# Kernel tuning notes

Measured on AMD Instinct MI355X. Metric: run time of the kernel, lower is better.

Reference implementation:

```python
import jax, jax.numpy as jnp
import numpy as np

TOPK = 180          # init kwarg topk
TOL = 3             # init kwarg tolerance_px


def setup_inputs() -> dict:
    key = jax.random.key(0)
    k1, k2, k3 = jax.random.split(key, 3)
    shape = (32, 1, 512, 512)
    return {
        "rv": jax.random.normal(k1, shape, dtype=jnp.float32),
        "ri": jax.random.normal(k2, shape, dtype=jnp.float32),
        "rf": jax.random.normal(k3, shape, dtype=jnp.float32),
    }


def reference(rv, ri, rf):
    # rf already matches rv spatially, so the interpolate branch is a no-op.
    b, c, h, w = rv.shape
    n = c * h * w
    rv_flat = rv.reshape(b, n)
    ri_flat = ri.reshape(b, n)
    rf_flat = rf.reshape(b, n)

    k = min(TOPK, n)
    _, rv_idx = jax.lax.top_k(rv_flat, k)                 # [b, k]
    _, ri_idx = jax.lax.top_k(ri_flat, k)                 # [b, k]
    _, rf_idx = jax.lax.top_k(rf_flat, min(2 * k, n))     # [b, 2k]

    rows = jnp.arange(b)[:, None]
    # union mask of VIS+IR keypoints (scatter 1.0 at top-k indices)
    src_mask = (
        jnp.zeros((b, n), jnp.float32)
        .at[rows, rv_idx].set(1.0)
        .at[rows, ri_idx].set(1.0)
    )
    src_mask = (src_mask > 0).astype(jnp.float32).reshape(b, c, h, w)

    fused_mask = (
        jnp.zeros((b, n), jnp.float32).at[rows, rf_idx].set(1.0)
    ).reshape(b, c, h, w)

    if TOL > 0:
        ksz = 2 * TOL + 1
        # max_pool2d(kernel=ksz, stride=1, padding=TOL) == dilation of the mask
        fused_mask = jax.lax.reduce_window(
            fused_mask, -jnp.inf, jax.lax.max,
            window_dimensions=(1, 1, ksz, ksz),
            window_strides=(1, 1, 1, 1),
            padding=[(0, 0), (0, 0), (TOL, TOL), (TOL, TOL)],
        )

    fused_hit = (fused_mask > 0).astype(jnp.float32)
    cover = (src_mask * fused_hit).reshape(b, -1).sum(axis=1)
    denom = jnp.maximum(src_mask.reshape(b, -1).sum(axis=1), 1.0)
    coverage = cover / denom
    return (1.0 - coverage).mean()
```

## Files before the change

### kernel.cpp

```cpp
#include <hip/hip_runtime.h>

#define N_ELEM 262144
#define SPLIT 32
#define NTS 256
#define SLICE_CAP 256
#define LSEL 2048
#define TIE_CAP 512
#define THRESH 2.5f

__device__ __forceinline__ unsigned keyOf(float f) {
    unsigned u = __float_as_uint(f);
    return (u & 0x80000000u) ? ~u : (u | 0x80000000u);
}

__device__ __forceinline__ const float* pairSrc(int p, const float* rv, const float* ri, const float* rf) {
    int t = p % 3, b = p / 3;
    return (t == 0 ? rv : (t == 1 ? ri : rf)) + (size_t)b * N_ELEM;
}

__global__ __launch_bounds__(NTS) void collect_kernel(const float* __restrict__ rv,
                                                      const float* __restrict__ ri,
                                                      const float* __restrict__ rf,
                                                      int* __restrict__ cntS,
                                                      unsigned long long* __restrict__ cand,
                                                      float* __restrict__ out,
                                                      int* __restrict__ done, int B) {
    const int p = blockIdx.x / SPLIT;
    const int s = blockIdx.x % SPLIT;
    const float4* p4 = (const float4*)pairSrc(p, rv, ri, rf) + (size_t)s * (N_ELEM / 4 / SPLIT);

    __shared__ unsigned long long buf[SLICE_CAP];
    __shared__ int s_m;
    const int tid = threadIdx.x;

    if (blockIdx.x == 0) {
        if (tid < B) done[tid] = 0;
        if (tid == B) *out = 0.0f;
    }
    if (tid == 0) s_m = 0;
    __syncthreads();

    const int base_idx = s * (N_ELEM / SPLIT);
    for (int i = tid; i < N_ELEM / 4 / SPLIT; i += NTS) {
        float4 v = p4[i];
        int pos;
        if (v.x > THRESH) { pos = atomicAdd(&s_m, 1); if (pos < SLICE_CAP) buf[pos] = ((unsigned long long)keyOf(v.x) << 32) | (unsigned)(base_idx + 4 * i + 0); }
        if (v.y > THRESH) { pos = atomicAdd(&s_m, 1); if (pos < SLICE_CAP) buf[pos] = ((unsigned long long)keyOf(v.y) << 32) | (unsigned)(base_idx + 4 * i + 1); }
        if (v.z > THRESH) { pos = atomicAdd(&s_m, 1); if (pos < SLICE_CAP) buf[pos] = ((unsigned long long)keyOf(v.z) << 32) | (unsigned)(base_idx + 4 * i + 2); }
        if (v.w > THRESH) { pos = atomicAdd(&s_m, 1); if (pos < SLICE_CAP) buf[pos] = ((unsigned long long)keyOf(v.w) << 32) | (unsigned)(base_idx + 4 * i + 3); }
    }
    __syncthreads();

    int m = s_m;
    const bool over = (m > SLICE_CAP);
    if (over) m = SLICE_CAP;
    if (tid == 0) cntS[p * SPLIT + s] = over ? -1 : m;
    unsigned long long* my = cand + (size_t)(p * SPLIT + s) * SLICE_CAP;
    for (int i = tid; i < m; i += NTS) my[i] = buf[i];
}

__global__ __launch_bounds__(NTS) void select_cov_kernel(const float* __restrict__ rv,
                                                         const float* __restrict__ ri,
                                                         const float* __restrict__ rf,
                                                         const int* __restrict__ cntS,
                                                         const unsigned long long* __restrict__ cand,
                                                         int* __restrict__ idx_out,
                                                         int* __restrict__ done,
                                                         float* __restrict__ out,
                                                         float inv_b) {
    const int p = blockIdx.x;
    const int t = p % 3;
    const int bb = p / 3;
    const int K = (t == 2) ? 360 : 180;
    int* obuf = idx_out + (size_t)p * 360;
    const int tid = threadIdx.x;

    __shared__ __align__(16) unsigned char smem[49152];
    unsigned* lcKey = (unsigned*)smem;
    unsigned* lcIdx = (unsigned*)(smem + 8192);
    __shared__ unsigned hist[256];
    __shared__ int ties[TIE_CAP];
    __shared__ int soff[SPLIT]; __shared__ int scnt[SPLIT];
    __shared__ int s_total, s_bad;
    __shared__ unsigned s_p2; __shared__ int s_b2; __shared__ int s_cg2;
    __shared__ int s_on, s_tn, s_pickd; __shared__ unsigned s_pickb;
    __shared__ int s_prev, s_u, s_c;

    if (tid < 64) {
        int c = (tid < SPLIT) ? cntS[p * SPLIT + tid] : 0;
        int bad = (c < 0) ? 1 : 0;
        int cc = bad ? 0 : c;
        int v = cc;
        #pragma unroll
        for (int off = 1; off < 64; off <<= 1) {
            int u = __shfl_up(v, off, 64);
            if (tid >= off) v += u;
        }
        if (tid < SPLIT) { soff[tid] = v - cc; scnt[tid] = cc; }
        if (tid == 63) s_total = v;
        unsigned long long bm = __ballot(bad != 0);
        if (tid == 0) s_bad = (bm != 0ull) ? 1 : 0;
    }
    __syncthreads();
    const int total = s_total;
    const bool fits = (!s_bad) && (total >= K) && (total <= LSEL);

    if (fits) {
        const int sl = tid >> 3;
        const int j0 = tid & 7;
        const unsigned long long* src = cand + (size_t)(p * SPLIT + sl) * SLICE_CAP;
        const int c = scnt[sl];
        const int o = soff[sl];
        for (int j = j0; j < c; j += 8) {
            unsigned long long e = src[j];
            lcKey[o + j] = (unsigned)(e >> 32);
            lcIdx[o + j] = (unsigned)(e & 0xffffffffu);
        }
    }
    __syncthreads();

    const float4* p4 = (const float4*)pairSrc(p, rv, ri, rf);

    if (tid == 0) { s_p2 = 0; s_b2 = 0; s_cg2 = 0; }
    __syncthreads();

    while (s_b2 < 32) {
        hist[tid] = 0;
        __syncthreads();
        {
            const int b2 = s_b2; const unsigned p2 = s_p2;
            const int sh2 = 24 - b2;
            if (fits) {
                for (int i = tid; i < total; i += NTS) {
                    unsigned kk = lcKey[i];
                    bool match = (b2 == 0) || ((kk >> (32 - b2)) == p2);
                    if (match) atomicAdd(&hist[(kk >> sh2) & 255u], 1u);
                }
            } else {
                for (int i = tid; i < N_ELEM / 4; i += NTS) {
                    float4 v = p4[i];
                    unsigned kk;
                    kk = keyOf(v.x); if ((b2 == 0) || ((kk >> (32 - b2)) == p2)) atomicAdd(&hist[(kk >> sh2) & 255u], 1u);
                    kk = keyOf(v.y); if ((b2 == 0) || ((kk >> (32 - b2)) == p2)) atomicAdd(&hist[(kk >> sh2) & 255u], 1u);
                    kk = keyOf(v.z); if ((b2 == 0) || ((kk >> (32 - b2)) == p2)) atomicAdd(&hist[(kk >> sh2) & 255u], 1u);
                    kk = keyOf(v.w); if ((b2 == 0) || ((kk >> (32 - b2)) == p2)) atomicAdd(&hist[(kk >> sh2) & 255u], 1u);
                }
            }
        }
        __syncthreads();
        const unsigned r = (unsigned)(K - s_cg2);
        if (tid < 64) {
            const int l = tid;
            unsigned h0 = hist[4*l+0], h1 = hist[4*l+1], h2 = hist[4*l+2], h3 = hist[4*l+3];
            unsigned sum4 = h0 + h1 + h2 + h3;
            unsigned suf = sum4;
            #pragma unroll
            for (int off = 1; off < 64; off <<= 1) {
                unsigned u = __shfl_down(suf, off, 64);
                if (l + off < 64) suf += u;
            }
            unsigned s0 = suf, s1 = s0 - h0, s2 = s1 - h1, s3 = s2 - h2, s4 = s3 - h3;
            int d = -1; unsigned below = 0;
            if      (s3 >= r && s4 < r) { d = 4*l+3; below = s4; }
            else if (s2 >= r && s3 < r) { d = 4*l+2; below = s3; }
            else if (s1 >= r && s2 < r) { d = 4*l+1; below = s2; }
            else if (s0 >= r && s1 < r) { d = 4*l+0; below = s1; }
            if (d >= 0) { s_pickd = d; s_pickb = below; }
        }
        __syncthreads();
        if (tid == 0) {
            s_p2 = (s_p2 << 8) | (unsigned)s_pickd;
            s_cg2 += (int)s_pickb;
            s_b2 += 8;
        }
        __syncthreads();
    }

    if (tid == 0) { s_on = 0; s_tn = 0; }
    __syncthreads();

    {
        const unsigned Kth = s_p2;
        if (fits) {
            for (int i = tid; i < total; i += NTS) {
                unsigned kk = lcKey[i];
                int idx = (int)lcIdx[i];
                if (kk > Kth) { int pos = atomicAdd(&s_on, 1); obuf[pos] = idx; }
                else if (kk == Kth) { int pos = atomicAdd(&s_tn, 1); if (pos < TIE_CAP) ties[pos] = idx; }
            }
        } else {
            for (int i = tid; i < N_ELEM / 4; i += NTS) {
                float4 v = p4[i];
                float vals[4] = {v.x, v.y, v.z, v.w};
                for (int c = 0; c < 4; ++c) {
                    unsigned kk = keyOf(vals[c]);
                    if (kk > Kth) { int pos = atomicAdd(&s_on, 1); obuf[pos] = 4 * i + c; }
                    else if (kk == Kth) { int pos = atomicAdd(&s_tn, 1); if (pos < TIE_CAP) ties[pos] = 4 * i + c; }
                }
            }
        }
    }
    __syncthreads();
    if (tid == 0) {
        int need = K - s_cg2;
        int tn = s_tn; if (tn > TIE_CAP) tn = TIE_CAP;
        int rr = need; if (rr > tn) rr = tn;
        for (int a = 0; a < rr; ++a) {
            int mb = a;
            for (int j = a + 1; j < tn; ++j) if (ties[j] < ties[mb]) mb = j;
            int tmp = ties[a]; ties[a] = ties[mb]; ties[mb] = tmp;
            obuf[s_on + a] = ties[a];
        }
        for (int a = rr; a < need; ++a) obuf[s_on + a] = (tn > 0) ? ties[0] : 0;
    }

    __threadfence();
    __syncthreads();
    if (tid == 0) s_prev = atomicAdd(&done[bb], 1);
    __syncthreads();
    if (s_prev == 2) {
        __threadfence();
        unsigned* rfbm  = (unsigned*)smem;
        unsigned* srcbm = (unsigned*)(smem + 32768);
        const int* rvI = idx_out + (size_t)(bb * 3 + 0) * 360;
        const int* riI = idx_out + (size_t)(bb * 3 + 1) * 360;
        const int* rfI = idx_out + (size_t)(bb * 3 + 2) * 360;

        for (int i = tid; i < 8192; i += NTS) rfbm[i] = 0;
        if (tid == 0) { s_u = 0; s_c = 0; }
        __syncthreads();
        for (int i = tid; i < 360; i += NTS) {
            int v = rfI[i];
            atomicOr(&rfbm[v >> 5], 1u << (v & 31));
        }
        __syncthreads();

        int myu = 0, myc = 0;
        for (int h = 0; h < 2; ++h) {
            for (int i = tid; i < 4096; i += NTS) srcbm[i] = 0;
            __syncthreads();
            for (int i = tid; i < 360; i += NTS) {
                int v = (i < 180) ? rvI[i] : riI[i - 180];
                int y = v >> 9, x = v & 511;
                if ((y >> 8) == h) {
                    unsigned bit = 1u << (v & 31);
                    unsigned old = atomicOr(&srcbm[(v >> 5) & 4095], bit);
                    if (!(old & bit)) {
                        myu++;
                        int lo = x - 3; if (lo < 0) lo = 0;
                        int hi = x + 3; if (hi > 511) hi = 511;
                        int k0 = lo >> 5, k1 = hi >> 5;
                        unsigned m0, m1;
                        if (k0 == k1) { m0 = ((1u << (hi - lo + 1)) - 1u) << (lo & 31); m1 = 0u; }
                        else          { m0 = 0xffffffffu << (lo & 31); m1 = (1u << ((hi & 31) + 1)) - 1u; }
                        unsigned cov = 0;
                        #pragma unroll
                        for (int dy = -3; dy <= 3; ++dy) {
                            int yy = y + dy;
                            if (yy >= 0 && yy < 512) {
                                const unsigned* row = &rfbm[yy << 4];
                                cov |= (row[k0] & m0);
                                if (k1 != k0) cov |= (row[k1] & m1);
                            }
                        }
                        myc += (cov != 0u) ? 1 : 0;
                    }
                }
            }
            __syncthreads();
        }
        if (myu) atomicAdd(&s_u, myu);
        if (myc) atomicAdd(&s_c, myc);
        __syncthreads();
        if (tid == 0) {
            float denom = (float)(s_u > 0 ? s_u : 1);
            float loss = 1.0f - (float)s_c / denom;
            atomicAdd(out, loss * inv_b);
        }
    }
}

extern "C" void kernel_launch(void* const* d_in, const int* in_sizes, int n_in,
                              void* d_out, int out_size, void* d_ws, size_t ws_size,
                              hipStream_t stream) {
    const float* rv = (const float*)d_in[0];
    const float* ri = (const float*)d_in[1];
    const float* rf = (const float*)d_in[2];
    float* out = (float*)d_out;

    const int B = in_sizes[0] / N_ELEM;
    const int P = 3 * B;

    char* ws = (char*)d_ws;
    int* cntS = (int*)ws;
    int* done = (int*)(ws + (size_t)P * SPLIT * 4);
    int* idx_buf = (int*)(ws + (size_t)P * SPLIT * 4 + (size_t)B * 4);
    size_t fixed = (size_t)P * SPLIT * 4 + (size_t)B * 4 + (size_t)P * 360 * 4;
    fixed = (fixed + 7) & ~(size_t)7;
    unsigned long long* cand = (unsigned long long*)(ws + fixed);

    collect_kernel<<<P * SPLIT, NTS, 0, stream>>>(rv, ri, rf, cntS, cand, out, done, B);
    select_cov_kernel<<<P, NTS, 0, stream>>>(rv, ri, rf, cntS, cand, idx_buf, done, out, 1.0f / (float)B);
}
```

Baseline: 143.8 us.

## Fuse collect and select kernels via last-block-done atomic counters

Result: slower. 529.1 us (+268.0%).

```diff
diff --git a/kernel.cpp b/kernel.cpp
--- a/kernel.cpp
+++ b/kernel.cpp
@@ -18,31 +18,51 @@
     return (t == 0 ? rv : (t == 1 ? ri : rf)) + (size_t)b * N_ELEM;
 }
 
-__global__ __launch_bounds__(NTS) void collect_kernel(const float* __restrict__ rv,
-                                                      const float* __restrict__ ri,
-                                                      const float* __restrict__ rf,
-                                                      int* __restrict__ cntS,
-                                                      unsigned long long* __restrict__ cand,
-                                                      float* __restrict__ out,
-                                                      int* __restrict__ done, int B) {
+__global__ void init_kernel(int* __restrict__ pairCnt, int P,
+                            int* __restrict__ batchCnt, int B,
+                            int* __restrict__ gcnt) {
+    int i = threadIdx.x;
+    for (int j = i; j < P; j += 256) pairCnt[j] = 0;
+    for (int j = i; j < B; j += 256) batchCnt[j] = 0;
+    if (i == 0) *gcnt = 0;
+}
+
+__global__ __launch_bounds__(NTS) void fused_kernel(const float* __restrict__ rv,
+                                                    const float* __restrict__ ri,
+                                                    const float* __restrict__ rf,
+                                                    int* __restrict__ cntS,
+                                                    unsigned long long* __restrict__ cand,
+                                                    int* __restrict__ idx_out,
+                                                    int* __restrict__ pairCnt,
+                                                    int* __restrict__ batchCnt,
+                                                    int* __restrict__ gcnt,
+                                                    float* __restrict__ lossArr,
+                                                    float* __restrict__ out,
+                                                    int B) {
     const int p = blockIdx.x / SPLIT;
     const int s = blockIdx.x % SPLIT;
-    const float4* p4 = (const float4*)pairSrc(p, rv, ri, rf) + (size_t)s * (N_ELEM / 4 / SPLIT);
-
-    __shared__ unsigned long long buf[SLICE_CAP];
-    __shared__ int s_m;
+    const int t = p % 3;
+    const int bb = p / 3;
+    const int K = (t == 2) ? 360 : 180;
     const int tid = threadIdx.x;
 
-    if (blockIdx.x == 0) {
-        if (tid < B) done[tid] = 0;
-        if (tid == B) *out = 0.0f;
-    }
+    __shared__ __align__(16) unsigned char smem[49152];
+    __shared__ unsigned hist[256];
+    __shared__ int ties[TIE_CAP];
+    __shared__ int soff[SPLIT]; __shared__ int scnt[SPLIT];
+    __shared__ int s_m, s_total, s_bad;
+    __shared__ unsigned s_p2; __shared__ int s_b2; __shared__ int s_cg2;
+    __shared__ int s_on, s_tn, s_pickd; __shared__ unsigned s_pickb;
+    __shared__ int s_last1, s_last2, s_last3;
+    __shared__ int s_u, s_c;
+
+    unsigned long long* buf = (unsigned long long*)smem;
     if (tid == 0) s_m = 0;
     __syncthreads();
-
+    const float4* p4s = (const float4*)pairSrc(p, rv, ri, rf) + (size_t)s * (N_ELEM / 4 / SPLIT);
     const int base_idx = s * (N_ELEM / SPLIT);
     for (int i = tid; i < N_ELEM / 4 / SPLIT; i += NTS) {
-        float4 v = p4[i];
+        float4 v = p4s[i];
         int pos;
         if (v.x > THRESH) { pos = atomicAdd(&s_m, 1); if (pos < SLICE_CAP) buf[pos] = ((unsigned long long)keyOf(v.x) << 32) | (unsigned)(base_idx + 4 * i + 0); }
         if (v.y > THRESH) { pos = atomicAdd(&s_m, 1); if (pos < SLICE_CAP) buf[pos] = ((unsigned long long)keyOf(v.y) << 32) | (unsigned)(base_idx + 4 * i + 1); }
@@ -50,41 +70,23 @@
         if (v.w > THRESH) { pos = atomicAdd(&s_m, 1); if (pos < SLICE_CAP) buf[pos] = ((unsigned long long)keyOf(v.w) << 32) | (unsigned)(base_idx + 4 * i + 3); }
     }
     __syncthreads();
-
-    int m = s_m;
-    const bool over = (m > SLICE_CAP);
-    if (over) m = SLICE_CAP;
-    if (tid == 0) cntS[p * SPLIT + s] = over ? -1 : m;
-    unsigned long long* my = cand + (size_t)(p * SPLIT + s) * SLICE_CAP;
-    for (int i = tid; i < m; i += NTS) my[i] = buf[i];
-}
-
-__global__ __launch_bounds__(NTS) void select_cov_kernel(const float* __restrict__ rv,
-                                                         const float* __restrict__ ri,
-                                                         const float* __restrict__ rf,
-                                                         const int* __restrict__ cntS,
-                                                         const unsigned long long* __restrict__ cand,
-                                                         int* __restrict__ idx_out,
-                                                         int* __restrict__ done,
-                                                         float* __restrict__ out,
-                                                         float inv_b) {
-    const int p = blockIdx.x;
-    const int t = p % 3;
-    const int bb = p / 3;
-    const int K = (t == 2) ? 360 : 180;
-    int* obuf = idx_out + (size_t)p * 360;
-    const int tid = threadIdx.x;
-
-    __shared__ __align__(16) unsigned char smem[49152];
+    {
+        int m = s_m;
+        const bool over = (m > SLICE_CAP);
+        if (over) m = SLICE_CAP;
+        if (tid == 0) cntS[p * SPLIT + s] = over ? -1 : m;
+        unsigned long long* myc = cand + (size_t)(p * SPLIT + s) * SLICE_CAP;
+        for (int i = tid; i < m; i += NTS) myc[i] = buf[i];
+    }
+    __threadfence();
+    __syncthreads();
+    if (tid == 0) s_last1 = (atomicAdd(&pairCnt[p], 1) == SPLIT - 1) ? 1 : 0;
+    __syncthreads();
+    if (!s_last1) return;
+
     unsigned* lcKey = (unsigned*)smem;
     unsigned* lcIdx = (unsigned*)(smem + 8192);
-    __shared__ unsigned hist[256];
-    __shared__ int ties[TIE_CAP];
-    __shared__ int soff[SPLIT]; __shared__ int scnt[SPLIT];
-    __shared__ int s_total, s_bad;
-    __shared__ unsigned s_p2; __shared__ int s_b2; __shared__ int s_cg2;
-    __shared__ int s_on, s_tn, s_pickd; __shared__ unsigned s_pickb;
-    __shared__ int s_prev, s_u, s_c;
+    int* obuf = idx_out + (size_t)p * 360;
 
     if (tid < 64) {
         int c = (tid < SPLIT) ? cntS[p * SPLIT + tid] : 0;
@@ -152,8 +154,7 @@
         if (tid < 64) {
             const int l = tid;
             unsigned h0 = hist[4*l+0], h1 = hist[4*l+1], h2 = hist[4*l+2], h3 = hist[4*l+3];
-            unsigned sum4 = h0 + h1 + h2 + h3;
-            unsigned suf = sum4;
+            unsigned suf = h0 + h1 + h2 + h3;
             #pragma unroll
             for (int off = 1; off < 64; off <<= 1) {
                 unsigned u = __shfl_down(suf, off, 64);
@@ -178,7 +179,6 @@
 
     if (tid == 0) { s_on = 0; s_tn = 0; }
     __syncthreads();
-
     {
         const unsigned Kth = s_p2;
         if (fits) {
@@ -216,10 +216,12 @@
 
     __threadfence();
     __syncthreads();
-    if (tid == 0) s_prev = atomicAdd(&done[bb], 1);
-    __syncthreads();
-    if (s_prev == 2) {
-        __threadfence();
+    if (tid == 0) s_last2 = (atomicAdd(&batchCnt[bb], 1) == 2) ? 1 : 0;
+    __syncthreads();
+    if (!s_last2) return;
+
+    __threadfence();
+    {
         unsigned* rfbm  = (unsigned*)smem;
         unsigned* srcbm = (unsigned*)(smem + 32768);
         const int* rvI = idx_out + (size_t)(bb * 3 + 0) * 360;
@@ -274,9 +276,22 @@
         __syncthreads();
         if (tid == 0) {
             float denom = (float)(s_u > 0 ? s_u : 1);
-            float loss = 1.0f - (float)s_c / denom;
-            atomicAdd(out, loss * inv_b);
-        }
+            ((volatile float*)lossArr)[bb] = 1.0f - (float)s_c / denom;
+        }
+    }
+    __threadfence();
+    __syncthreads();
+    if (tid == 0) s_last3 = (atomicAdd(gcnt, 1) == B - 1) ? 1 : 0;
+    __syncthreads();
+    if (!s_last3) return;
+
+    __threadfence();
+    if (tid < 64) {
+        float v = 0.0f;
+        for (int j = tid; j < B; j += 64) v += ((volatile float*)lossArr)[j];
+        #pragma unroll
+        for (int off = 32; off; off >>= 1) v += __shfl_down(v, off, 64);
+        if (tid == 0) *out = v / (float)B;
     }
 }
 
@@ -292,13 +307,17 @@
     const int P = 3 * B;
 
     char* ws = (char*)d_ws;
-    int* cntS = (int*)ws;
-    int* done = (int*)(ws + (size_t)P * SPLIT * 4);
-    int* idx_buf = (int*)(ws + (size_t)P * SPLIT * 4 + (size_t)B * 4);
-    size_t fixed = (size_t)P * SPLIT * 4 + (size_t)B * 4 + (size_t)P * 360 * 4;
+    int* cntS     = (int*)ws;
+    int* pairCnt  = cntS + (size_t)P * SPLIT;
+    int* batchCnt = pairCnt + P;
+    int* gcnt     = batchCnt + B;
+    float* lossArr = (float*)(gcnt + 1);
+    int* idx_buf  = (int*)(lossArr + B);
+    size_t fixed = (size_t)((char*)(idx_buf + (size_t)P * 360) - ws);
     fixed = (fixed + 7) & ~(size_t)7;
     unsigned long long* cand = (unsigned long long*)(ws + fixed);
 
-    collect_kernel<<<P * SPLIT, NTS, 0, stream>>>(rv, ri, rf, cntS, cand, out, done, B);
-    select_cov_kernel<<<P, NTS, 0, stream>>>(rv, ri, rf, cntS, cand, idx_buf, done, out, 1.0f / (float)B);
-}
+    init_kernel<<<1, 256, 0, stream>>>(pairCnt, P, batchCnt, B, gcnt);
+    fused_kernel<<<P * SPLIT, NTS, 0, stream>>>(rv, ri, rf, cntS, cand, idx_buf,
+                                                pairCnt, batchCnt, gcnt, lossArr, out, B);
+}
```
